# Kernel optimization log

Hardware: AMD Instinct MI355X
Metric: run time of the kernel (lower is better)

Reference implementation:

```python
import jax, jax.numpy as jnp
import numpy as np

B, LQ, LD, H, C = 128, 32, 512, 768, 128


def setup_inputs() -> dict:
    key = jax.random.key(0)
    ks = jax.random.split(key, 8)
    return {
        "query_hidden": jax.random.normal(ks[0], (B, LQ, H), dtype=jnp.float32),
        "doc_hidden": jax.random.normal(ks[1], (B, LD, H), dtype=jnp.float32),
        "query_mask": jax.random.randint(ks[2], (B, LQ), 0, 2, dtype=jnp.int32),
        "doc_mask": jax.random.randint(ks[3], (B, LD), 0, 2, dtype=jnp.int32),
        "W_comp": jax.random.normal(ks[4], (H, C), dtype=jnp.float32) * (1.0 / np.sqrt(H)),
        "b_comp": jax.random.normal(ks[5], (C,), dtype=jnp.float32) * 0.02,
        "w_stop": jax.random.normal(ks[6], (C, 1), dtype=jnp.float32) * (1.0 / np.sqrt(C)),
        "b_stop": jnp.ones((1,), dtype=jnp.float32),  # nn.init.constant_(bias, 1)
        "score_merger": jnp.zeros((1,), dtype=jnp.float32),
    }


def reference(query_hidden, doc_hidden, query_mask, doc_mask,
              W_comp, b_comp, w_stop, b_stop, score_merger):
    qm = query_mask.astype(bool)  # [B, LQ]
    dm = doc_mask.astype(bool)    # [B, LD]

    # encode_shared: CLS vec is the UNcompressed hidden state at position 0
    q_cls = query_hidden[:, 0, :]  # [B, H]
    d_cls = doc_hidden[:, 0, :]    # [B, H]

    # compressor (Linear H->C)
    q_vecs = jnp.einsum('blh,hc->blc', query_hidden, W_comp) + b_comp  # [B, LQ, C]
    d_tok = jnp.einsum('blh,hc->blc', doc_hidden, W_comp) + b_comp     # [B, LD, C]

    # encode_query: zero masked query tokens
    q_vecs = q_vecs * qm[..., None]

    # encode_doc: stopword reducer (relu of Linear C->1), then importance + mask
    importance = jax.nn.relu(jnp.einsum('blc,co->blo', d_tok, w_stop) + b_stop)  # [B, LD, 1]
    d_vecs = d_tok * importance * dm[..., None]

    # CLS score: dot product of (uncompressed) CLS vectors
    cls_score = jnp.sum(q_cls * d_cls, axis=-1)  # [B]

    # term score: MaxSim over doc tokens, masked sum over query tokens
    scores = jnp.einsum('bqc,bkc->bqk', q_vecs, d_vecs)      # [B, LQ, LD]
    scores = jnp.where(dm[:, None, :], scores, -1000.0)
    term = jnp.max(scores, axis=-1)                          # [B, LQ]
    term_score = jnp.sum(jnp.where(qm, term, 0.0), axis=-1)  # [B]

    w = jax.nn.sigmoid(score_merger[0])
    cls_score = cls_score * w
    term_score = term_score * (1.0 - w)
    score = cls_score + term_score
    return (score, cls_score, term_score)
```

## Files before the change

kernel.cpp:

```cpp
#include <hip/hip_runtime.h>
#include <hip/hip_bf16.h>

#define Bb 128
#define LQ 32
#define LD 512
#define Hh 768
#define Cc 128

#define DBLOCKS ((Bb * LD) / 64)
#define QBLOCKS ((Bb * LQ) / 64)

typedef short bf16x8 __attribute__((ext_vector_type(8)));
typedef short bf16x4 __attribute__((ext_vector_type(4)));
typedef float f32x4 __attribute__((ext_vector_type(4)));

__device__ __forceinline__ short f2bf(float f) {
  union { float f; unsigned u; } v;
  v.f = f;
  unsigned u = v.u + (0x7FFFu + ((v.u >> 16) & 1u));
  return (short)(u >> 16);
}

__global__ __launch_bounds__(256) void k_wt(const float* __restrict__ W,
                                            short* __restrict__ Wt) {
  int idx = blockIdx.x * 256 + threadIdx.x;
  int h = idx >> 7;
  int c = idx & 127;
  Wt[c * Hh + h] = f2bf(W[idx]);
}

__global__ __launch_bounds__(256, 4) void k_proj_q(
    const float* __restrict__ qh, const short* __restrict__ Wt,
    const float* __restrict__ bcomp, const int* __restrict__ qmask,
    float* __restrict__ qv) {
  constexpr int ASTR = 144;
  constexpr int BSTR = 160;
  constexpr int ASZ = 64 * ASTR;
  constexpr int BSZ = 128 * BSTR;
  __shared__ __align__(16) char sm[ASZ + BSZ];

  const int tid = threadIdx.x;
  const int w = tid >> 6;
  const int lane = tid & 63;
  const int quad = lane >> 4;
  const int lm = lane & 15;

  const long row0b = (long)blockIdx.x * 64;

  const float* gA = qh + (row0b + w * 16 + (lane >> 4)) * (long)Hh + (lane & 15) * 4;
  const short* gB = Wt + (w * 32 + (lane >> 3)) * Hh + (lane & 7) * 8;
  const int aoff = (w * 16 + (lane >> 4)) * ASTR + (lane & 15) * 8;
  const int boff = (w * 32 + (lane >> 3)) * BSTR + (lane & 7) * 16;

  char* bufA = sm;
  char* bufB = sm + ASZ;

  f32x4 acc[8];
#pragma unroll
  for (int j = 0; j < 8; ++j) acc[j] = (f32x4){0.f, 0.f, 0.f, 0.f};

  float4 ar[4];
  bf16x8 br[4];
#pragma unroll
  for (int i = 0; i < 4; ++i) ar[i] = *(const float4*)(gA + i * 4 * Hh);
#pragma unroll
  for (int i = 0; i < 4; ++i) br[i] = *(const bf16x8*)(gB + i * 8 * Hh);

  for (int kk = 0; kk < Hh / 64; ++kk) {
    __syncthreads();
#pragma unroll
    for (int i = 0; i < 4; ++i) {
      bf16x4 p;
      p[0] = f2bf(ar[i].x); p[1] = f2bf(ar[i].y);
      p[2] = f2bf(ar[i].z); p[3] = f2bf(ar[i].w);
      *(bf16x4*)(bufA + aoff + i * 4 * ASTR) = p;
    }
#pragma unroll
    for (int i = 0; i < 4; ++i)
      *(bf16x8*)(bufB + boff + i * 8 * BSTR) = br[i];
    __syncthreads();

    {
      const long go = (kk + 1 < Hh / 64) ? (long)(kk + 1) * 64 : 0;
#pragma unroll
      for (int i = 0; i < 4; ++i) ar[i] = *(const float4*)(gA + i * 4 * Hh + go);
#pragma unroll
      for (int i = 0; i < 4; ++i) br[i] = *(const bf16x8*)(gB + i * 8 * Hh + go);
    }

#pragma unroll
    for (int ks = 0; ks < 2; ++ks) {
      bf16x8 fa = *(const bf16x8*)(bufA + (w * 16 + lm) * ASTR + ks * 64 + quad * 16);
#pragma unroll
      for (int j = 0; j < 8; ++j) {
        bf16x8 fb = *(const bf16x8*)(bufB + (j * 16 + lm) * BSTR + ks * 64 + quad * 16);
        acc[j] = __builtin_amdgcn_mfma_f32_16x16x32_bf16(fa, fb, acc[j], 0, 0, 0);
      }
    }
  }

  const long row0 = row0b + w * 16;
  float bc[8];
#pragma unroll
  for (int j = 0; j < 8; ++j) bc[j] = bcomp[j * 16 + lm];

#pragma unroll
  for (int r = 0; r < 4; ++r) {
    const long row = row0 + quad * 4 + r;
    const float scale = (float)qmask[row];
    float* yr = qv + row * Cc;
#pragma unroll
    for (int j = 0; j < 8; ++j) yr[j * 16 + lm] = (acc[j][r] + bc[j]) * scale;
  }
}

__global__ __launch_bounds__(256, 3) void k_doc_score(
    const float* __restrict__ dh, const short* __restrict__ Wt,
    const float* __restrict__ bcomp, const int* __restrict__ dmask,
    const float* __restrict__ wstop, const float* __restrict__ bstop,
    const float* __restrict__ qv, float* __restrict__ partial) {
  constexpr int ASTR = 144;
  constexpr int BSTR = 160;
  constexpr int ASZ = 64 * ASTR;
  constexpr int BSZ = 128 * BSTR;
  __shared__ __align__(16) char sm[ASZ + BSZ];
  __shared__ float lq[LQ][Cc + 4];
  __shared__ float pm[LQ][4];

  const int tid = threadIdx.x;
  const int w = tid >> 6;
  const int lane = tid & 63;
  const int quad = lane >> 4;
  const int lm = lane & 15;

  const int b = blockIdx.x >> 3;
  const int chunk = blockIdx.x & 7;
  const long row0b = (long)b * LD + chunk * 64;

  {
    const float4* src = (const float4*)(qv + (size_t)b * LQ * Cc);
    for (int i = tid; i < LQ * Cc / 4; i += 256) {
      float4 v = src[i];
      int q = i >> 5;
      int c = (i & 31) << 2;
      *(float4*)&lq[q][c] = v;
    }
  }

  const float* gA = dh + (row0b + w * 16 + (lane >> 4)) * (long)Hh + (lane & 15) * 4;
  const short* gB = Wt + (w * 32 + (lane >> 3)) * Hh + (lane & 7) * 8;
  const int aoff = (w * 16 + (lane >> 4)) * ASTR + (lane & 15) * 8;
  const int boff = (w * 32 + (lane >> 3)) * BSTR + (lane & 7) * 16;

  char* bufA = sm;
  char* bufB = sm + ASZ;

  f32x4 acc[8];
#pragma unroll
  for (int j = 0; j < 8; ++j) acc[j] = (f32x4){0.f, 0.f, 0.f, 0.f};

  float4 ar[4];
  bf16x8 br[4];
#pragma unroll
  for (int i = 0; i < 4; ++i) ar[i] = *(const float4*)(gA + i * 4 * Hh);
#pragma unroll
  for (int i = 0; i < 4; ++i) br[i] = *(const bf16x8*)(gB + i * 8 * Hh);

  for (int kk = 0; kk < Hh / 64; ++kk) {
    __syncthreads();
#pragma unroll
    for (int i = 0; i < 4; ++i) {
      bf16x4 p;
      p[0] = f2bf(ar[i].x); p[1] = f2bf(ar[i].y);
      p[2] = f2bf(ar[i].z); p[3] = f2bf(ar[i].w);
      *(bf16x4*)(bufA + aoff + i * 4 * ASTR) = p;
    }
#pragma unroll
    for (int i = 0; i < 4; ++i)
      *(bf16x8*)(bufB + boff + i * 8 * BSTR) = br[i];
    __syncthreads();

    {
      const long go = (kk + 1 < Hh / 64) ? (long)(kk + 1) * 64 : 0;
#pragma unroll
      for (int i = 0; i < 4; ++i) ar[i] = *(const float4*)(gA + i * 4 * Hh + go);
#pragma unroll
      for (int i = 0; i < 4; ++i) br[i] = *(const bf16x8*)(gB + i * 8 * Hh + go);
    }

#pragma unroll
    for (int ks = 0; ks < 2; ++ks) {
      bf16x8 fa = *(const bf16x8*)(bufA + (w * 16 + lm) * ASTR + ks * 64 + quad * 16);
#pragma unroll
      for (int j = 0; j < 8; ++j) {
        bf16x8 fb = *(const bf16x8*)(bufB + (j * 16 + lm) * BSTR + ks * 64 + quad * 16);
        acc[j] = __builtin_amdgcn_mfma_f32_16x16x32_bf16(fa, fb, acc[j], 0, 0, 0);
      }
    }
  }

  const long row0 = row0b + w * 16;
  float bc[8], wsv[8];
#pragma unroll
  for (int j = 0; j < 8; ++j) bc[j] = bcomp[j * 16 + lm];
#pragma unroll
  for (int j = 0; j < 8; ++j) wsv[j] = wstop[j * 16 + lm];
  const float bs = bstop[0];

  float vv[4][8];
  int rm[4];
#pragma unroll
  for (int r = 0; r < 4; ++r) {
    const long row = row0 + quad * 4 + r;
    float v[8];
#pragma unroll
    for (int j = 0; j < 8; ++j) v[j] = acc[j][r] + bc[j];
    float p = 0.f;
#pragma unroll
    for (int j = 0; j < 8; ++j) p += v[j] * wsv[j];
    p += __shfl_xor(p, 1);
    p += __shfl_xor(p, 2);
    p += __shfl_xor(p, 4);
    p += __shfl_xor(p, 8);
    const float imp = fmaxf(p + bs, 0.f);
    const int m = dmask[row];
    rm[r] = m;
    const float scale = imp * (float)m;
#pragma unroll
    for (int j = 0; j < 8; ++j) vv[r][j] = v[j] * scale;
  }

#pragma unroll
  for (int qo = 0; qo < LQ; qo += 4) {
#pragma unroll
    for (int qi = 0; qi < 4; ++qi) {
      const int q = qo + qi;
      float ql[8];
#pragma unroll
      for (int j = 0; j < 8; ++j) ql[j] = lq[q][j * 16 + lm];
      float mx = -1000.f;
#pragma unroll
      for (int r = 0; r < 4; ++r) {
        float p = 0.f;
#pragma unroll
        for (int j = 0; j < 8; ++j) p += ql[j] * vv[r][j];
        p += __shfl_xor(p, 1);
        p += __shfl_xor(p, 2);
        p += __shfl_xor(p, 4);
        p += __shfl_xor(p, 8);
        const float s = rm[r] ? p : -1000.f;
        mx = fmaxf(mx, s);
      }
      mx = fmaxf(mx, __shfl_xor(mx, 16));
      mx = fmaxf(mx, __shfl_xor(mx, 32));
      if (lane == 0) pm[q][w] = mx;
    }
  }
  __syncthreads();
  if (tid < LQ) {
    float mx = fmaxf(fmaxf(pm[tid][0], pm[tid][1]), fmaxf(pm[tid][2], pm[tid][3]));
    partial[((size_t)b * LQ + tid) * 8 + chunk] = mx;
  }
}

__global__ __launch_bounds__(256) void k_final(
    const float* __restrict__ qh, const float* __restrict__ dh,
    const int* __restrict__ qmask, const float* __restrict__ partial,
    const float* __restrict__ merger, float* __restrict__ out) {
  const int b = blockIdx.x;
  const int tid = threadIdx.x;
  __shared__ float red[256];
  __shared__ float clss;
  const float* qc = qh + (size_t)b * LQ * Hh;
  const float* dc = dh + (size_t)b * LD * Hh;
  float s = 0.f;
  for (int h = tid; h < Hh; h += 256) s += qc[h] * dc[h];
  red[tid] = s;
  __syncthreads();
  for (int off = 128; off > 0; off >>= 1) {
    if (tid < off) red[tid] += red[tid + off];
    __syncthreads();
  }
  if (tid == 0) clss = red[0];
  __syncthreads();
  float t = 0.f;
  if (tid < LQ) {
    const float* pp = partial + ((size_t)b * LQ + tid) * 8;
    float mx = pp[0];
#pragma unroll
    for (int c = 1; c < 8; ++c) mx = fmaxf(mx, pp[c]);
    if (qmask[b * LQ + tid]) t = mx;
  }
  red[tid] = t;
  __syncthreads();
  for (int off = 128; off > 0; off >>= 1) {
    if (tid < off) red[tid] += red[tid + off];
    __syncthreads();
  }
  if (tid == 0) {
    float w = 1.f / (1.f + expf(-merger[0]));
    float cs = clss * w;
    float ts = red[0] * (1.f - w);
    out[b] = cs + ts;
    out[Bb + b] = cs;
    out[2 * Bb + b] = ts;
  }
}

extern "C" void kernel_launch(void* const* d_in, const int* in_sizes, int n_in,
                              void* d_out, int out_size, void* d_ws, size_t ws_size,
                              hipStream_t stream) {
  const float* qh  = (const float*)d_in[0];
  const float* dh  = (const float*)d_in[1];
  const int*   qm  = (const int*)d_in[2];
  const int*   dm  = (const int*)d_in[3];
  const float* W   = (const float*)d_in[4];
  const float* bc  = (const float*)d_in[5];
  const float* wst = (const float*)d_in[6];
  const float* bst = (const float*)d_in[7];
  const float* mrg = (const float*)d_in[8];
  float* out = (float*)d_out;

  char* ws = (char*)d_ws;
  short* Wt  = (short*)ws;
  float* qv  = (float*)(ws + 196608);
  float* prt = (float*)(ws + 196608 + 2097152);

  k_wt<<<(Hh * Cc) / 256, 256, 0, stream>>>(W, Wt);
  k_proj_q<<<QBLOCKS, 256, 0, stream>>>(qh, Wt, bc, qm, qv);
  k_doc_score<<<DBLOCKS, 256, 0, stream>>>(dh, Wt, bc, dm, wst, bst, qv, prt);
  k_final<<<Bb, 256, 0, stream>>>(qh, dh, qm, prt, mrg, out);
}
```

Before: 350.8 us.

## Stage doc vectors in LDS and compute MaxSim with register-tiled dot products

The doc-token vectors are written to shared memory, which reuses the GEMM staging buffer, and the doc mask is cached there too. The shuffle-heavy per-query MaxSim reduction is replaced by a 2x4 register-tiled query-by-doc dot-product loop over LDS, followed by a 16-way max reduction. This removes the many cross-lane shuffles and the replicated per-wave work in the epilogue. In exchange it adds LDS traffic and extra barriers, and changes shared-memory usage, which may affect occupancy.

```diff
diff --git a/kernel.cpp b/kernel.cpp
--- a/kernel.cpp
+++ b/kernel.cpp
@@ -123,9 +123,16 @@
   constexpr int BSTR = 160;
   constexpr int ASZ = 64 * ASTR;
   constexpr int BSZ = 128 * BSTR;
-  __shared__ __align__(16) char sm[ASZ + BSZ];
-  __shared__ float lq[LQ][Cc + 4];
-  __shared__ float pm[LQ][4];
+  constexpr int DSTR = 132;
+  constexpr int DVB = 64 * DSTR * 4;
+  __shared__ __align__(16) char smem[DVB + 32 * DSTR * 4 + 256 + 2048];
+
+  char* bufA = smem;
+  char* bufB = smem + ASZ;
+  float* dvt = (float*)smem;
+  float* lqt = (float*)(smem + DVB);
+  int* dmsk = (int*)(smem + DVB + 32 * DSTR * 4);
+  float* pm = (float*)(smem + DVB + 32 * DSTR * 4 + 256);
 
   const int tid = threadIdx.x;
   const int w = tid >> 6;
@@ -143,17 +150,15 @@
       float4 v = src[i];
       int q = i >> 5;
       int c = (i & 31) << 2;
-      *(float4*)&lq[q][c] = v;
-    }
-  }
+      *(float4*)&lqt[q * DSTR + c] = v;
+    }
+  }
+  if (tid < 64) dmsk[tid] = dmask[row0b + tid];
 
   const float* gA = dh + (row0b + w * 16 + (lane >> 4)) * (long)Hh + (lane & 15) * 4;
   const short* gB = Wt + (w * 32 + (lane >> 3)) * Hh + (lane & 7) * 8;
   const int aoff = (w * 16 + (lane >> 4)) * ASTR + (lane & 15) * 8;
   const int boff = (w * 32 + (lane >> 3)) * BSTR + (lane & 7) * 16;
-
-  char* bufA = sm;
-  char* bufB = sm + ASZ;
 
   f32x4 acc[8];
 #pragma unroll
@@ -199,7 +204,8 @@
     }
   }
 
-  const long row0 = row0b + w * 16;
+  __syncthreads();
+
   float bc[8], wsv[8];
 #pragma unroll
   for (int j = 0; j < 8; ++j) bc[j] = bcomp[j * 16 + lm];
@@ -207,11 +213,9 @@
   for (int j = 0; j < 8; ++j) wsv[j] = wstop[j * 16 + lm];
   const float bs = bstop[0];
 
-  float vv[4][8];
-  int rm[4];
 #pragma unroll
   for (int r = 0; r < 4; ++r) {
-    const long row = row0 + quad * 4 + r;
+    const int lrow = w * 16 + quad * 4 + r;
     float v[8];
 #pragma unroll
     for (int j = 0; j < 8; ++j) v[j] = acc[j][r] + bc[j];
@@ -223,42 +227,52 @@
     p += __shfl_xor(p, 4);
     p += __shfl_xor(p, 8);
     const float imp = fmaxf(p + bs, 0.f);
-    const int m = dmask[row];
-    rm[r] = m;
-    const float scale = imp * (float)m;
-#pragma unroll
-    for (int j = 0; j < 8; ++j) vv[r][j] = v[j] * scale;
-  }
-
-#pragma unroll
-  for (int qo = 0; qo < LQ; qo += 4) {
-#pragma unroll
-    for (int qi = 0; qi < 4; ++qi) {
-      const int q = qo + qi;
-      float ql[8];
-#pragma unroll
-      for (int j = 0; j < 8; ++j) ql[j] = lq[q][j * 16 + lm];
-      float mx = -1000.f;
-#pragma unroll
-      for (int r = 0; r < 4; ++r) {
-        float p = 0.f;
-#pragma unroll
-        for (int j = 0; j < 8; ++j) p += ql[j] * vv[r][j];
-        p += __shfl_xor(p, 1);
-        p += __shfl_xor(p, 2);
-        p += __shfl_xor(p, 4);
-        p += __shfl_xor(p, 8);
-        const float s = rm[r] ? p : -1000.f;
-        mx = fmaxf(mx, s);
-      }
-      mx = fmaxf(mx, __shfl_xor(mx, 16));
-      mx = fmaxf(mx, __shfl_xor(mx, 32));
-      if (lane == 0) pm[q][w] = mx;
-    }
-  }
+    const float scale = imp * (float)dmsk[lrow];
+#pragma unroll
+    for (int j = 0; j < 8; ++j) dvt[lrow * DSTR + j * 16 + lm] = v[j] * scale;
+  }
+  __syncthreads();
+
+  const int qt = tid & 15;
+  const int kt = tid >> 4;
+  const int kbase = kt * 4;
+  float a[2][4];
+#pragma unroll
+  for (int qi = 0; qi < 2; ++qi)
+#pragma unroll
+    for (int ki = 0; ki < 4; ++ki) a[qi][ki] = 0.f;
+
+  for (int c = 0; c < Cc; c += 4) {
+    float4 q0 = *(float4*)&lqt[qt * DSTR + c];
+    float4 q1 = *(float4*)&lqt[(qt + 16) * DSTR + c];
+    float4 d0 = *(float4*)&dvt[(kbase + 0) * DSTR + c];
+    float4 d1 = *(float4*)&dvt[(kbase + 1) * DSTR + c];
+    float4 d2 = *(float4*)&dvt[(kbase + 2) * DSTR + c];
+    float4 d3 = *(float4*)&dvt[(kbase + 3) * DSTR + c];
+    a[0][0] += q0.x * d0.x + q0.y * d0.y + q0.z * d0.z + q0.w * d0.w;
+    a[0][1] += q0.x * d1.x + q0.y * d1.y + q0.z * d1.z + q0.w * d1.w;
+    a[0][2] += q0.x * d2.x + q0.y * d2.y + q0.z * d2.z + q0.w * d2.w;
+    a[0][3] += q0.x * d3.x + q0.y * d3.y + q0.z * d3.z + q0.w * d3.w;
+    a[1][0] += q1.x * d0.x + q1.y * d0.y + q1.z * d0.z + q1.w * d0.w;
+    a[1][1] += q1.x * d1.x + q1.y * d1.y + q1.z * d1.z + q1.w * d1.w;
+    a[1][2] += q1.x * d2.x + q1.y * d2.y + q1.z * d2.z + q1.w * d2.w;
+    a[1][3] += q1.x * d3.x + q1.y * d3.y + q1.z * d3.z + q1.w * d3.w;
+  }
+  float m0 = -1000.f, m1 = -1000.f;
+#pragma unroll
+  for (int ki = 0; ki < 4; ++ki) {
+    if (dmsk[kbase + ki]) {
+      m0 = fmaxf(m0, a[0][ki]);
+      m1 = fmaxf(m1, a[1][ki]);
+    }
+  }
+  pm[qt * 16 + kt] = m0;
+  pm[(qt + 16) * 16 + kt] = m1;
   __syncthreads();
   if (tid < LQ) {
-    float mx = fmaxf(fmaxf(pm[tid][0], pm[tid][1]), fmaxf(pm[tid][2], pm[tid][3]));
+    float mx = pm[tid * 16];
+#pragma unroll
+    for (int t = 1; t < 16; ++t) mx = fmaxf(mx, pm[tid * 16 + t]);
     partial[((size_t)b * LQ + tid) * 8 + chunk] = mx;
   }
 }
```

Result: faster. 331.3 us (-5.6%).
